# Kernel optimization log

Hardware: AMD Instinct MI355X
Metric: run time of the kernel (lower is better)

Reference implementation:

```python
import jax, jax.numpy as jnp
import numpy as np


def setup_inputs() -> dict:
    key = jax.random.key(0)
    ks = jax.random.split(key, 8)
    B, A = 2048, 64
    STATE, ACT = 5, 4
    d_in = STATE + ACT  # 9
    x = jax.random.normal(ks[0], (B, STATE), dtype=jnp.float32)
    actions = jax.random.normal(ks[1], (A, ACT), dtype=jnp.float32)
    def lin(k, fin, fout):
        return jax.random.normal(k, (fin, fout), dtype=jnp.float32) / np.sqrt(fin)
    W1 = lin(ks[2], d_in, 128); b1 = jnp.zeros((128,), jnp.float32)
    W2 = lin(ks[3], 128, 1024); b2 = jnp.zeros((1024,), jnp.float32)
    W3 = lin(ks[4], 1024, 1024); b3 = jnp.zeros((1024,), jnp.float32)
    W4 = lin(ks[5], 1024, 128); b4 = jnp.zeros((128,), jnp.float32)
    W5 = lin(ks[6], 128, 1); b5 = jnp.zeros((1,), jnp.float32)
    return {"x": x, "actions": actions,
            "W1": W1, "b1": b1, "W2": W2, "b2": b2, "W3": W3, "b3": b3,
            "W4": W4, "b4": b4, "W5": W5, "b5": b5}


def reference(x, actions, W1, b1, W2, b2, W3, b3, W4, b4, W5, b5):
    # x: [B,5] states; actions: [A,4] candidate actions.
    # Equivalent to the original's per-sample per-action loop: evaluate the
    # 5-layer Tanh MLP on concat(state, action) for every (sample, action) pair.
    B = x.shape[0]
    A = actions.shape[0]
    s = jnp.broadcast_to(x[:, None, :], (B, A, x.shape[1]))
    a = jnp.broadcast_to(actions[None, :, :], (B, A, actions.shape[1]))
    inp = jnp.concatenate([s, a], axis=-1)  # [B,A,9]
    h = jnp.tanh(inp @ W1 + b1)
    h = jnp.tanh(h @ W2 + b2)
    h = jnp.tanh(h @ W3 + b3)
    h = jnp.tanh(h @ W4 + b4)
    values = (h @ W5 + b5)[..., 0]  # [B,A]
    best = jnp.argmax(values, axis=1)  # [B]
    max_value_action = actions[best]  # [B,4]
    return (max_value_action, values)
```

## Files before the change

kernel.cpp:

```cpp
#include <hip/hip_runtime.h>
#include <hip/hip_bf16.h>
#include <math.h>


typedef short bf16x8 __attribute__((ext_vector_type(8)));
typedef float f32x4 __attribute__((ext_vector_type(4)));
typedef float f32x16 __attribute__((ext_vector_type(16)));

__device__ __host__ inline unsigned short f2bf(float f) {
    union { float f; unsigned u; } v; v.f = f;
    unsigned r = v.u + 0x7fff + ((v.u >> 16) & 1);
    return (unsigned short)(r >> 16);
}
__device__ inline unsigned short cvt_bf16(float f) {
    __hip_bfloat16 h = __float2bfloat16(f);
    return *reinterpret_cast<unsigned short*>(&h);
}
__device__ inline float bf2f(unsigned short b) {
    union { unsigned u; float f; } v; v.u = ((unsigned)b) << 16;
    return v.f;
}
__device__ inline float fast_tanh(float x) {
    float e = __expf(2.0f * x);
    return 1.0f - 2.0f * __builtin_amdgcn_rcpf(e + 1.0f);
}

#define DELTA 0.025f
#define WL_CAP 4096

struct WLE { unsigned long long mask; unsigned s; unsigned pad; };

#define HSWZ(row, b) ((b) ^ (((row) & 15) << 4))

__global__ __launch_bounds__(256) void pack_all(
    const float* __restrict__ W2, const float* __restrict__ W3, const float* __restrict__ W4,
    unsigned short* __restrict__ W2p, unsigned short* __restrict__ W3p,
    unsigned short* __restrict__ W4p, unsigned* __restrict__ wl_cnt)
{
    int tid = blockIdx.x * 256 + threadIdx.x;
    if (tid == 0) *wl_cnt = 0u;
    int blob = tid >> 6, lane = tid & 63;
    if (blob >= 2560) return;
    bf16x8 v;
    if (blob < 256) {
        int nt = blob >> 2, kt = blob & 3;
        int n = nt * 16 + (lane & 15);
        int kbase = kt * 32 + ((lane >> 4) & 3) * 8;
        #pragma unroll
        for (int e = 0; e < 8; ++e) v[e] = (short)f2bf(W2[(size_t)(kbase + e) * 1024 + n]);
        *(bf16x8*)&W2p[(size_t)blob * 512 + lane * 8] = v;
    } else if (blob < 2304) {
        int lb = blob - 256;
        int nt = lb >> 6, kt = lb & 63;
        int n = nt * 32 + (lane & 31);
        int kbase = kt * 16 + (lane >> 5) * 8;
        #pragma unroll
        for (int e = 0; e < 8; ++e) v[e] = (short)f2bf(W3[(size_t)(kbase + e) * 1024 + n]);
        *(bf16x8*)&W3p[(size_t)lb * 512 + lane * 8] = v;
    } else {
        int lb = blob - 2304;
        int nt = lb >> 5, kt = lb & 31;
        int n = nt * 16 + (lane & 15);
        int kbase = kt * 32 + ((lane >> 4) & 3) * 8;
        #pragma unroll
        for (int e = 0; e < 8; ++e) v[e] = (short)f2bf(W4[(size_t)(kbase + e) * 128 + n]);
        *(bf16x8*)&W4p[(size_t)lb * 512 + lane * 8] = v;
    }
}

__global__ __launch_bounds__(1024, 4) void qnet_mfma(
    const float* __restrict__ x, const float* __restrict__ actions,
    const float* __restrict__ W1, const float* __restrict__ b1,
    const float* __restrict__ b2, const float* __restrict__ b3,
    const float* __restrict__ b4,
    const float* __restrict__ W5, const float* __restrict__ b5,
    const unsigned short* __restrict__ W2p,
    const unsigned short* __restrict__ W3p,
    const unsigned short* __restrict__ W4p,
    float* __restrict__ values)
{
    __shared__ unsigned short h2b[2][64 * 256];
    __shared__ unsigned short hc[64 * 128];

    const int t = threadIdx.x;
    const int lane = t & 63;
    const int wave = t >> 6;
    const int p0 = blockIdx.x * 64;
    const int l15 = lane & 15;
    const int kb16 = (lane >> 4) * 16;
    const int kb32 = (lane >> 5) * 16;

    {
        int r = t >> 4;
        int c0 = (t & 15) * 8;
        const float* xs = &x[blockIdx.x * 5];
        const float* as = &actions[r * 4];
        float in[9] = { xs[0], xs[1], xs[2], xs[3], xs[4], as[0], as[1], as[2], as[3] };
        #pragma unroll
        for (int j = 0; j < 8; ++j) {
            int c = c0 + j;
            float acc = b1[c];
            #pragma unroll
            for (int k = 0; k < 9; ++k) acc += in[k] * W1[k * 128 + c];
            *(unsigned short*)((char*)hc + r * 256 + HSWZ(r, c * 2)) = cvt_bf16(fast_tanh(acc));
        }
    }
    __syncthreads();

    auto layer2_chunk = [&](int c, int buf) {
        const int nT = c * 16 + wave;
        const float bv = b2[nT * 16 + l15];
        char* bufp = (char*)&h2b[buf][0];
        const int lcb = (nT & 15) * 32 + l15 * 2;
        #pragma unroll 1
        for (int rt = 0; rt < 4; ++rt) {
            f32x4 acc = (f32x4){ bv, bv, bv, bv };
            const int row = rt * 16 + l15;
            #pragma unroll
            for (int ks = 0; ks < 4; ++ks) {
                bf16x8 b = *(const bf16x8*)((const char*)W2p + (nT * 4 + ks) * 1024 + lane * 16);
                bf16x8 a = *(const bf16x8*)((const char*)hc + row * 256 + HSWZ(row, ks * 64 + kb16));
                acc = __builtin_amdgcn_mfma_f32_16x16x32_bf16(a, b, acc, 0, 0, 0);
            }
            #pragma unroll
            for (int rr = 0; rr < 4; ++rr) {
                int m = rt * 16 + (lane >> 4) * 4 + rr;
                *(unsigned short*)(bufp + m * 512 + HSWZ(m, lcb)) = cvt_bf16(fast_tanh(acc[rr]));
            }
        }
    };

    f32x16 a00, a01, a10, a11;
    {
        float bv0 = b3[wave * 64 + (lane & 31)];
        float bv1 = b3[wave * 64 + 32 + (lane & 31)];
        #pragma unroll
        for (int i = 0; i < 16; ++i) { a00[i] = bv0; a10[i] = bv0; a01[i] = bv1; a11[i] = bv1; }
    }

    layer2_chunk(0, 0);
    __syncthreads();

    const int r0 = lane & 31, r1 = 32 + (lane & 31);
    for (int c = 0; c < 4; ++c) {
        if (c < 3) layer2_chunk(c + 1, (c + 1) & 1);
        const char* buf = (const char*)&h2b[c & 1][0];
        const char* bb = (const char*)W3p + (wave * 128 + c * 16) * 1024 + lane * 16;
        #pragma unroll 2
        for (int kt = 0; kt < 16; ++kt) {
            bf16x8 A0 = *(const bf16x8*)(buf + r0 * 512 + HSWZ(r0, kt * 32 + kb32));
            bf16x8 A1 = *(const bf16x8*)(buf + r1 * 512 + HSWZ(r1, kt * 32 + kb32));
            bf16x8 B0 = *(const bf16x8*)(bb + kt * 1024);
            bf16x8 B1 = *(const bf16x8*)(bb + 65536 + kt * 1024);
            a00 = __builtin_amdgcn_mfma_f32_32x32x16_bf16(A0, B0, a00, 0, 0, 0);
            a10 = __builtin_amdgcn_mfma_f32_32x32x16_bf16(A1, B0, a10, 0, 0, 0);
            a01 = __builtin_amdgcn_mfma_f32_32x32x16_bf16(A0, B1, a01, 0, 0, 0);
            a11 = __builtin_amdgcn_mfma_f32_32x32x16_bf16(A1, B1, a11, 0, 0, 0);
        }
        __syncthreads();
    }

    char* stage = (char*)&h2b[0][0];
    const int ct = wave & 7, rtp = wave >> 3;
    const int c0b = (wave * 64 + (lane & 31)) * 2;
    const float bv4 = b4[ct * 16 + l15];

    #pragma unroll
    for (int h = 0; h < 2; ++h) {
        #pragma unroll
        for (int r = 0; r < 16; ++r) {
            int row = (r & 3) + 8 * (r >> 2) + 4 * (lane >> 5);
            float vlo = h ? a10[r] : a00[r];
            float vhi = h ? a11[r] : a01[r];
            *(unsigned short*)(stage + row * 2048 + HSWZ(row, c0b)) = cvt_bf16(fast_tanh(vlo));
            *(unsigned short*)(stage + row * 2048 + HSWZ(row, c0b + 64)) = cvt_bf16(fast_tanh(vhi));
        }
        __syncthreads();
        f32x4 acc4 = (f32x4){ bv4, bv4, bv4, bv4 };
        const int rowL = rtp * 16 + l15;
        #pragma unroll 4
        for (int k32 = 0; k32 < 32; ++k32) {
            bf16x8 B = *(const bf16x8*)((const char*)W4p + (ct * 32 + k32) * 1024 + lane * 16);
            bf16x8 a = *(const bf16x8*)(stage + rowL * 2048 + HSWZ(rowL, k32 * 64 + kb16));
            acc4 = __builtin_amdgcn_mfma_f32_16x16x32_bf16(a, B, acc4, 0, 0, 0);
        }
        int n = ct * 16 + l15;
        #pragma unroll
        for (int rr = 0; rr < 4; ++rr) {
            int m = h * 32 + rtp * 16 + (lane >> 4) * 4 + rr;
            *(unsigned short*)((char*)hc + m * 256 + HSWZ(m, n * 2)) = cvt_bf16(fast_tanh(acc4[rr]));
        }
        __syncthreads();
    }

    {
        int r = t >> 4, g = t & 15;
        float part = 0.0f;
        #pragma unroll
        for (int j = 0; j < 8; ++j) {
            int cidx = g * 8 + j;
            unsigned short hb = *(const unsigned short*)((const char*)hc + r * 256 + HSWZ(r, cidx * 2));
            part += bf2f(hb) * W5[cidx];
        }
        part += __shfl_down(part, 8);
        part += __shfl_down(part, 4);
        part += __shfl_down(part, 2);
        part += __shfl_down(part, 1);
        if (g == 0) values[p0 + r] = part + b5[0];
    }
}

__global__ __launch_bounds__(256) void scan_argmax(
    const float* __restrict__ values, const float* __restrict__ actions,
    float* __restrict__ out_actions, unsigned* __restrict__ wl_cnt,
    WLE* __restrict__ wl)
{
    int wave = threadIdx.x >> 6, lane = threadIdx.x & 63;
    int s = blockIdx.x * 4 + wave;
    float myv = values[s * 64 + lane];
    float v = myv; int idx = lane;
    #pragma unroll
    for (int off = 32; off; off >>= 1) {
        float ov = __shfl_down(v, off);
        int oi = __shfl_down(idx, off);
        if (ov > v || (ov == v && oi < idx)) { v = ov; idx = oi; }
    }
    float vm = __shfl(v, 0);
    int best = __shfl(idx, 0);
    unsigned long long mask = __ballot(myv >= vm - DELTA);
    if (lane == 0 && __popcll(mask) > 1) {
        unsigned slot = atomicAdd(wl_cnt, 1u);
        if (slot < WL_CAP) { wl[slot].mask = mask; wl[slot].s = (unsigned)s; }
    }
    if (lane < 4) out_actions[s * 4 + lane] = actions[best * 4 + lane];
}

__global__ __launch_bounds__(256) void fixup_eval(
    const float* __restrict__ x, const float* __restrict__ actions,
    const float* __restrict__ W1, const float* __restrict__ b1,
    const float* __restrict__ W2, const float* __restrict__ b2,
    const float* __restrict__ W3, const float* __restrict__ b3,
    const float* __restrict__ W4, const float* __restrict__ b4,
    const float* __restrict__ W5, const float* __restrict__ b5,
    const unsigned* __restrict__ wl_cnt, const WLE* __restrict__ wl,
    float* __restrict__ out_actions)
{
    __shared__ float h1s[8][128];
    __shared__ float h2s[8][1024];
    __shared__ float h3s[8][1024];
    __shared__ float h4s[8][128];
    __shared__ float ain[8][4];
    __shared__ float xs[5];
    __shared__ int cand[64];
    __shared__ int ncand;
    __shared__ float vals[8];
    __shared__ float bestv; __shared__ int besti;

    const int t = threadIdx.x;
    int n = (int)*wl_cnt;
    if (n > WL_CAP) n = WL_CAP;
    for (int e = blockIdx.x; e < n; e += gridDim.x) {
        unsigned long long mask = wl[e].mask;
        int s = (int)wl[e].s;
        if (t == 0) {
            int nn = 0; unsigned long long m2 = mask;
            while (m2) { cand[nn++] = __ffsll(m2) - 1; m2 &= m2 - 1; }
            ncand = nn; bestv = -1e30f; besti = 0;
        }
        if (t < 5) xs[t] = x[s * 5 + t];
        __syncthreads();
        const int NC = ncand;
        for (int g = 0; g < NC; g += 8) {
            if (t < 32) {
                int rr = t >> 2;
                int src = (g + rr < NC) ? cand[g + rr] : cand[g];
                ain[rr][t & 3] = actions[src * 4 + (t & 3)];
            }
            __syncthreads();
            {
                int r = t >> 5, cb = (t & 31) * 4;
                #pragma unroll
                for (int j = 0; j < 4; ++j) {
                    int c = cb + j;
                    float acc = b1[c];
                    #pragma unroll
                    for (int k = 0; k < 5; ++k) acc += xs[k] * W1[k * 128 + c];
                    #pragma unroll
                    for (int k = 0; k < 4; ++k) acc += ain[r][k] * W1[(5 + k) * 128 + c];
                    h1s[r][c] = tanhf(acc);
                }
            }
            __syncthreads();
            {
                int cb = t * 4;
                float acc[8][4];
                float4 bv = *(const float4*)&b2[cb];
                #pragma unroll
                for (int r = 0; r < 8; ++r) { acc[r][0]=bv.x; acc[r][1]=bv.y; acc[r][2]=bv.z; acc[r][3]=bv.w; }
                for (int k = 0; k < 128; ++k) {
                    float4 w = *(const float4*)&W2[k * 1024 + cb];
                    #pragma unroll
                    for (int r = 0; r < 8; ++r) {
                        float hv = h1s[r][k];
                        acc[r][0] += hv * w.x; acc[r][1] += hv * w.y;
                        acc[r][2] += hv * w.z; acc[r][3] += hv * w.w;
                    }
                }
                #pragma unroll
                for (int r = 0; r < 8; ++r) {
                    h2s[r][cb+0] = tanhf(acc[r][0]); h2s[r][cb+1] = tanhf(acc[r][1]);
                    h2s[r][cb+2] = tanhf(acc[r][2]); h2s[r][cb+3] = tanhf(acc[r][3]);
                }
            }
            __syncthreads();
            {
                int cb = t * 4;
                float acc[8][4];
                float4 bv = *(const float4*)&b3[cb];
                #pragma unroll
                for (int r = 0; r < 8; ++r) { acc[r][0]=bv.x; acc[r][1]=bv.y; acc[r][2]=bv.z; acc[r][3]=bv.w; }
                for (int k = 0; k < 1024; ++k) {
                    float4 w = *(const float4*)&W3[k * 1024 + cb];
                    #pragma unroll
                    for (int r = 0; r < 8; ++r) {
                        float hv = h2s[r][k];
                        acc[r][0] += hv * w.x; acc[r][1] += hv * w.y;
                        acc[r][2] += hv * w.z; acc[r][3] += hv * w.w;
                    }
                }
                #pragma unroll
                for (int r = 0; r < 8; ++r) {
                    h3s[r][cb+0] = tanhf(acc[r][0]); h3s[r][cb+1] = tanhf(acc[r][1]);
                    h3s[r][cb+2] = tanhf(acc[r][2]); h3s[r][cb+3] = tanhf(acc[r][3]);
                }
            }
            __syncthreads();
            {
                int r = t >> 5, cb = (t & 31) * 4;
                float acc[4];
                float4 bv = *(const float4*)&b4[cb];
                acc[0]=bv.x; acc[1]=bv.y; acc[2]=bv.z; acc[3]=bv.w;
                for (int k = 0; k < 1024; ++k) {
                    float4 w = *(const float4*)&W4[k * 128 + cb];
                    float hv = h3s[r][k];
                    acc[0] += hv * w.x; acc[1] += hv * w.y; acc[2] += hv * w.z; acc[3] += hv * w.w;
                }
                h4s[r][cb+0] = tanhf(acc[0]); h4s[r][cb+1] = tanhf(acc[1]);
                h4s[r][cb+2] = tanhf(acc[2]); h4s[r][cb+3] = tanhf(acc[3]);
            }
            __syncthreads();
            if (t < 8) {
                float acc = b5[0];
                for (int k = 0; k < 128; ++k) acc += h4s[t][k] * W5[k];
                vals[t] = acc;
            }
            __syncthreads();
            if (t == 0) {
                int lim = (NC - g < 8) ? (NC - g) : 8;
                for (int i = 0; i < lim; ++i)
                    if (vals[i] > bestv) { bestv = vals[i]; besti = cand[g + i]; }
            }
            __syncthreads();
        }
        if (t < 4) out_actions[s * 4 + t] = actions[besti * 4 + t];
        __syncthreads();
    }
}

#define TR 16
__global__ __launch_bounds__(256) void qnet_fused(
    const float* __restrict__ x, const float* __restrict__ actions,
    const float* __restrict__ W1, const float* __restrict__ b1,
    const float* __restrict__ W2, const float* __restrict__ b2,
    const float* __restrict__ W3, const float* __restrict__ b3,
    const float* __restrict__ W4, const float* __restrict__ b4,
    const float* __restrict__ W5, const float* __restrict__ b5,
    float* __restrict__ values)
{
    __shared__ float h_small[TR][128];
    __shared__ float hA[TR][1024];
    __shared__ float hB[TR][1024];
    const int t = threadIdx.x;
    const int p0 = blockIdx.x * TR;
    for (int i = t; i < TR * 128; i += 256) {
        int r = i >> 7, c = i & 127;
        int p = p0 + r;
        int bidx = p >> 6, aidx = p & 63;
        float acc = b1[c];
        for (int k = 0; k < 5; ++k) acc += x[bidx * 5 + k] * W1[k * 128 + c];
        for (int k = 0; k < 4; ++k) acc += actions[aidx * 4 + k] * W1[(5 + k) * 128 + c];
        h_small[r][c] = tanhf(acc);
    }
    __syncthreads();
    {
        const int c0 = t * 4;
        float4 bias = *(const float4*)&b2[c0];
        float acc[TR][4];
        for (int r = 0; r < TR; ++r) { acc[r][0]=bias.x; acc[r][1]=bias.y; acc[r][2]=bias.z; acc[r][3]=bias.w; }
        for (int k = 0; k < 128; k += 4) {
            float4 w0 = *(const float4*)&W2[(k+0)*1024+c0];
            float4 w1 = *(const float4*)&W2[(k+1)*1024+c0];
            float4 w2 = *(const float4*)&W2[(k+2)*1024+c0];
            float4 w3 = *(const float4*)&W2[(k+3)*1024+c0];
            for (int r = 0; r < TR; ++r) {
                float4 hv = *(const float4*)&h_small[r][k];
                acc[r][0] += hv.x*w0.x + hv.y*w1.x + hv.z*w2.x + hv.w*w3.x;
                acc[r][1] += hv.x*w0.y + hv.y*w1.y + hv.z*w2.y + hv.w*w3.y;
                acc[r][2] += hv.x*w0.z + hv.y*w1.z + hv.z*w2.z + hv.w*w3.z;
                acc[r][3] += hv.x*w0.w + hv.y*w1.w + hv.z*w2.w + hv.w*w3.w;
            }
        }
        for (int r = 0; r < TR; ++r) {
            hA[r][c0+0]=tanhf(acc[r][0]); hA[r][c0+1]=tanhf(acc[r][1]);
            hA[r][c0+2]=tanhf(acc[r][2]); hA[r][c0+3]=tanhf(acc[r][3]);
        }
    }
    __syncthreads();
    {
        const int c0 = t * 4;
        float4 bias = *(const float4*)&b3[c0];
        float acc[TR][4];
        for (int r = 0; r < TR; ++r) { acc[r][0]=bias.x; acc[r][1]=bias.y; acc[r][2]=bias.z; acc[r][3]=bias.w; }
        for (int k = 0; k < 1024; k += 4) {
            float4 w0 = *(const float4*)&W3[(k+0)*1024+c0];
            float4 w1 = *(const float4*)&W3[(k+1)*1024+c0];
            float4 w2 = *(const float4*)&W3[(k+2)*1024+c0];
            float4 w3 = *(const float4*)&W3[(k+3)*1024+c0];
            for (int r = 0; r < TR; ++r) {
                float4 hv = *(const float4*)&hA[r][k];
                acc[r][0] += hv.x*w0.x + hv.y*w1.x + hv.z*w2.x + hv.w*w3.x;
                acc[r][1] += hv.x*w0.y + hv.y*w1.y + hv.z*w2.y + hv.w*w3.y;
                acc[r][2] += hv.x*w0.z + hv.y*w1.z + hv.z*w2.z + hv.w*w3.z;
                acc[r][3] += hv.x*w0.w + hv.y*w1.w + hv.z*w2.w + hv.w*w3.w;
            }
        }
        for (int r = 0; r < TR; ++r) {
            hB[r][c0+0]=tanhf(acc[r][0]); hB[r][c0+1]=tanhf(acc[r][1]);
            hB[r][c0+2]=tanhf(acc[r][2]); hB[r][c0+3]=tanhf(acc[r][3]);
        }
    }
    __syncthreads();
    {
        const int c = t & 127;
        const int rh = t >> 7;
        float acc[8];
        float bias = b4[c];
        for (int r = 0; r < 8; ++r) acc[r] = bias;
        for (int k = 0; k < 1024; k += 4) {
            float w0 = W4[(k+0)*128+c], w1 = W4[(k+1)*128+c];
            float w2 = W4[(k+2)*128+c], w3 = W4[(k+3)*128+c];
            for (int r = 0; r < 8; ++r) {
                float4 hv = *(const float4*)&hB[rh*8+r][k];
                acc[r] += hv.x*w0 + hv.y*w1 + hv.z*w2 + hv.w*w3;
            }
        }
        for (int r = 0; r < 8; ++r) h_small[rh*8+r][c] = tanhf(acc[r]);
    }
    __syncthreads();
    if (t < TR) {
        float acc = b5[0];
        for (int k = 0; k < 128; k += 4) {
            float4 hv = *(const float4*)&h_small[t][k];
            float4 wv = *(const float4*)&W5[k];
            acc += hv.x*wv.x + hv.y*wv.y + hv.z*wv.z + hv.w*wv.w;
        }
        values[p0 + t] = acc;
    }
}

__global__ __launch_bounds__(256) void argmax_gather(
    const float* __restrict__ values, const float* __restrict__ actions,
    float* __restrict__ out_actions)
{
    const int wave = threadIdx.x >> 6;
    const int lane = threadIdx.x & 63;
    const int state = blockIdx.x * (blockDim.x >> 6) + wave;
    float v = values[state * 64 + lane];
    int idx = lane;
    for (int off = 32; off; off >>= 1) {
        float ov = __shfl_down(v, off);
        int oi = __shfl_down(idx, off);
        if (ov > v || (ov == v && oi < idx)) { v = ov; idx = oi; }
    }
    idx = __shfl(idx, 0);
    if (lane < 4) out_actions[state * 4 + lane] = actions[idx * 4 + lane];
}

extern "C" void kernel_launch(void* const* d_in, const int* in_sizes, int n_in,
                              void* d_out, int out_size, void* d_ws, size_t ws_size,
                              hipStream_t stream) {
    const float* x       = (const float*)d_in[0];
    const float* actions = (const float*)d_in[1];
    const float* W1 = (const float*)d_in[2];  const float* b1 = (const float*)d_in[3];
    const float* W2 = (const float*)d_in[4];  const float* b2 = (const float*)d_in[5];
    const float* W3 = (const float*)d_in[6];  const float* b3 = (const float*)d_in[7];
    const float* W4 = (const float*)d_in[8];  const float* b4 = (const float*)d_in[9];
    const float* W5 = (const float*)d_in[10]; const float* b5 = (const float*)d_in[11];

    float* out_actions = (float*)d_out;
    float* values      = (float*)d_out + 2048 * 4;

    const size_t nW2 = 128 * 1024, nW3 = 1024 * 1024, nW4 = 1024 * 128;
    const size_t wbytes = (nW2 + nW3 + nW4) * sizeof(unsigned short);
    const size_t need = wbytes + 16 + (size_t)WL_CAP * sizeof(WLE);

    if (ws_size >= need) {
        unsigned short* W2p = (unsigned short*)d_ws;
        unsigned short* W3p = W2p + nW2;
        unsigned short* W4p = W3p + nW3;
        unsigned* wl_cnt = (unsigned*)((char*)d_ws + wbytes);
        WLE* wl = (WLE*)((char*)d_ws + wbytes + 16);

        pack_all<<<640, 256, 0, stream>>>(W2, W3, W4, W2p, W3p, W4p, wl_cnt);
        qnet_mfma<<<2048, 1024, 0, stream>>>(x, actions, W1, b1, b2, b3, b4, W5, b5,
                                             W2p, W3p, W4p, values);
        scan_argmax<<<512, 256, 0, stream>>>(values, actions, out_actions, wl_cnt, wl);
        fixup_eval<<<512, 256, 0, stream>>>(x, actions, W1, b1, W2, b2, W3, b3,
                                            W4, b4, W5, b5, wl_cnt, wl, out_actions);
    } else {
        qnet_fused<<<2048 * 64 / TR, 256, 0, stream>>>(x, actions, W1, b1, W2, b2, W3, b3,
                                                       W4, b4, W5, b5, values);
        argmax_gather<<<2048 / 4, 256, 0, stream>>>(values, actions, out_actions);
    }
}
```

Measured before the change: 643.6 us.

## Halve qnet block to 512 threads, split layer3 into two passes, rework fixup

The main MFMA kernel now uses 8 waves instead of 16. Each wave computes two layer-2 column tiles, and layer 3 runs in two output-column passes. Layer 4 partial sums accumulate across both passes, so layer 2 is computed twice per block. This frees LDS staging space and could allow higher occupancy per CU, and s_setprio is added around the layer-3 MFMA loop. In exchange, each wave does more serial work and layer 2 is redundantly recomputed. The fixup kernel is also changed to 1024-thread blocks with one output column per thread.

```diff
diff --git a/kernel.cpp b/kernel.cpp
--- a/kernel.cpp
+++ b/kernel.cpp
@@ -68,7 +68,7 @@
     }
 }
 
-__global__ __launch_bounds__(1024, 4) void qnet_mfma(
+__global__ __launch_bounds__(512, 4) void qnet_mfma(
     const float* __restrict__ x, const float* __restrict__ actions,
     const float* __restrict__ W1, const float* __restrict__ b1,
     const float* __restrict__ b2, const float* __restrict__ b3,
@@ -79,25 +79,25 @@
     const unsigned short* __restrict__ W4p,
     float* __restrict__ values)
 {
-    __shared__ unsigned short h2b[2][64 * 256];
+    __shared__ unsigned short h2b[2 * 64 * 256];
     __shared__ unsigned short hc[64 * 128];
 
     const int t = threadIdx.x;
     const int lane = t & 63;
-    const int wave = t >> 6;
+    const int w = t >> 6;
     const int p0 = blockIdx.x * 64;
     const int l15 = lane & 15;
     const int kb16 = (lane >> 4) * 16;
     const int kb32 = (lane >> 5) * 16;
 
     {
-        int r = t >> 4;
-        int c0 = (t & 15) * 8;
+        int r = t >> 3;
+        int c0 = (t & 7) * 16;
         const float* xs = &x[blockIdx.x * 5];
         const float* as = &actions[r * 4];
         float in[9] = { xs[0], xs[1], xs[2], xs[3], xs[4], as[0], as[1], as[2], as[3] };
-        #pragma unroll
-        for (int j = 0; j < 8; ++j) {
+        #pragma unroll 4
+        for (int j = 0; j < 16; ++j) {
             int c = c0 + j;
             float acc = b1[c];
             #pragma unroll
@@ -107,102 +107,133 @@
     }
     __syncthreads();
 
-    auto layer2_chunk = [&](int c, int buf) {
-        const int nT = c * 16 + wave;
-        const float bv = b2[nT * 16 + l15];
-        char* bufp = (char*)&h2b[buf][0];
-        const int lcb = (nT & 15) * 32 + l15 * 2;
+    auto layer2_chunk = [&](int c, int b) {
+        char* bufp = (char*)h2b + b * 32768;
+        #pragma unroll
+        for (int j = 0; j < 2; ++j) {
+            const int nT = c * 16 + w * 2 + j;
+            const float bv = b2[nT * 16 + l15];
+            const int lcb = ((w * 2 + j) * 16 + l15) * 2;
+            #pragma unroll 1
+            for (int rt = 0; rt < 4; ++rt) {
+                f32x4 acc = (f32x4){ bv, bv, bv, bv };
+                const int row = rt * 16 + l15;
+                #pragma unroll
+                for (int ks = 0; ks < 4; ++ks) {
+                    bf16x8 bfr = *(const bf16x8*)((const char*)W2p + (nT * 4 + ks) * 1024 + lane * 16);
+                    bf16x8 a = *(const bf16x8*)((const char*)hc + row * 256 + HSWZ(row, ks * 64 + kb16));
+                    acc = __builtin_amdgcn_mfma_f32_16x16x32_bf16(a, bfr, acc, 0, 0, 0);
+                }
+                #pragma unroll
+                for (int rr = 0; rr < 4; ++rr) {
+                    int m = rt * 16 + (lane >> 4) * 4 + rr;
+                    *(unsigned short*)(bufp + m * 512 + HSWZ(m, lcb)) = cvt_bf16(fast_tanh(acc[rr]));
+                }
+            }
+        }
+    };
+
+    f32x4 acc4[4];
+    {
+        const float bv4 = b4[w * 16 + l15];
+        #pragma unroll
+        for (int rt = 0; rt < 4; ++rt) acc4[rt] = (f32x4){ bv4, bv4, bv4, bv4 };
+    }
+
+    layer2_chunk(0, 0);
+    __syncthreads();
+
+    const int r0 = lane & 31, r1 = 32 + (lane & 31);
+
+    #pragma unroll 1
+    for (int p = 0; p < 2; ++p) {
+        f32x16 a00, a01, a10, a11;
+        {
+            float bv0 = b3[p * 512 + w * 64 + (lane & 31)];
+            float bv1 = b3[p * 512 + w * 64 + 32 + (lane & 31)];
+            #pragma unroll
+            for (int i = 0; i < 16; ++i) { a00[i] = bv0; a10[i] = bv0; a01[i] = bv1; a11[i] = bv1; }
+        }
+        const int bbase = ((p * 16 + w * 2) * 64) * 1024 + lane * 16;
+
         #pragma unroll 1
-        for (int rt = 0; rt < 4; ++rt) {
-            f32x4 acc = (f32x4){ bv, bv, bv, bv };
-            const int row = rt * 16 + l15;
+        for (int c = 0; c < 4; ++c) {
+            if (c < 3) layer2_chunk(c + 1, (c + 1) & 1);
+            const char* bufp = (const char*)h2b + (c & 1) * 32768;
+            const char* bb = (const char*)W3p + bbase + c * 16384;
+            __builtin_amdgcn_s_setprio(1);
+            #pragma unroll 2
+            for (int kt = 0; kt < 16; ++kt) {
+                bf16x8 A0 = *(const bf16x8*)(bufp + r0 * 512 + HSWZ(r0, kt * 32 + kb32));
+                bf16x8 A1 = *(const bf16x8*)(bufp + r1 * 512 + HSWZ(r1, kt * 32 + kb32));
+                bf16x8 B0 = *(const bf16x8*)(bb + kt * 1024);
+                bf16x8 B1 = *(const bf16x8*)(bb + 65536 + kt * 1024);
+                a00 = __builtin_amdgcn_mfma_f32_32x32x16_bf16(A0, B0, a00, 0, 0, 0);
+                a10 = __builtin_amdgcn_mfma_f32_32x32x16_bf16(A1, B0, a10, 0, 0, 0);
+                a01 = __builtin_amdgcn_mfma_f32_32x32x16_bf16(A0, B1, a01, 0, 0, 0);
+                a11 = __builtin_amdgcn_mfma_f32_32x32x16_bf16(A1, B1, a11, 0, 0, 0);
+            }
+            __builtin_amdgcn_s_setprio(0);
+            __syncthreads();
+        }
+
+        {
+            char* stage = (char*)h2b;
+            const int lc0 = (w * 64 + (lane & 31)) * 2;
             #pragma unroll
-            for (int ks = 0; ks < 4; ++ks) {
-                bf16x8 b = *(const bf16x8*)((const char*)W2p + (nT * 4 + ks) * 1024 + lane * 16);
-                bf16x8 a = *(const bf16x8*)((const char*)hc + row * 256 + HSWZ(row, ks * 64 + kb16));
-                acc = __builtin_amdgcn_mfma_f32_16x16x32_bf16(a, b, acc, 0, 0, 0);
-            }
+            for (int r = 0; r < 16; ++r) {
+                int row = (r & 3) + 8 * (r >> 2) + 4 * (lane >> 5);
+                int rowB = row + 32;
+                *(unsigned short*)(stage + row  * 1024 + HSWZ(row,  lc0)) = cvt_bf16(fast_tanh(a00[r]));
+                *(unsigned short*)(stage + rowB * 1024 + HSWZ(rowB, lc0)) = cvt_bf16(fast_tanh(a10[r]));
+                *(unsigned short*)(stage + row  * 1024 + HSWZ(row,  lc0 + 64)) = cvt_bf16(fast_tanh(a01[r]));
+                *(unsigned short*)(stage + rowB * 1024 + HSWZ(rowB, lc0 + 64)) = cvt_bf16(fast_tanh(a11[r]));
+            }
+        }
+        __syncthreads();
+
+        {
+            const char* stage = (const char*)h2b;
+            #pragma unroll 2
+            for (int kg = 0; kg < 16; ++kg) {
+                bf16x8 B = *(const bf16x8*)((const char*)W4p + (w * 32 + p * 16 + kg) * 1024 + lane * 16);
+                #pragma unroll
+                for (int rt = 0; rt < 4; ++rt) {
+                    int row = rt * 16 + l15;
+                    bf16x8 a = *(const bf16x8*)(stage + row * 1024 + HSWZ(row, kg * 64 + kb16));
+                    acc4[rt] = __builtin_amdgcn_mfma_f32_16x16x32_bf16(a, B, acc4[rt], 0, 0, 0);
+                }
+            }
+        }
+        __syncthreads();
+
+        if (p == 0) {
+            layer2_chunk(0, 0);
+            __syncthreads();
+        }
+    }
+
+    {
+        int n = w * 16 + l15;
+        #pragma unroll
+        for (int rt = 0; rt < 4; ++rt)
             #pragma unroll
             for (int rr = 0; rr < 4; ++rr) {
                 int m = rt * 16 + (lane >> 4) * 4 + rr;
-                *(unsigned short*)(bufp + m * 512 + HSWZ(m, lcb)) = cvt_bf16(fast_tanh(acc[rr]));
-            }
-        }
-    };
-
-    f32x16 a00, a01, a10, a11;
-    {
-        float bv0 = b3[wave * 64 + (lane & 31)];
-        float bv1 = b3[wave * 64 + 32 + (lane & 31)];
-        #pragma unroll
-        for (int i = 0; i < 16; ++i) { a00[i] = bv0; a10[i] = bv0; a01[i] = bv1; a11[i] = bv1; }
-    }
-
-    layer2_chunk(0, 0);
-    __syncthreads();
-
-    const int r0 = lane & 31, r1 = 32 + (lane & 31);
-    for (int c = 0; c < 4; ++c) {
-        if (c < 3) layer2_chunk(c + 1, (c + 1) & 1);
-        const char* buf = (const char*)&h2b[c & 1][0];
-        const char* bb = (const char*)W3p + (wave * 128 + c * 16) * 1024 + lane * 16;
-        #pragma unroll 2
-        for (int kt = 0; kt < 16; ++kt) {
-            bf16x8 A0 = *(const bf16x8*)(buf + r0 * 512 + HSWZ(r0, kt * 32 + kb32));
-            bf16x8 A1 = *(const bf16x8*)(buf + r1 * 512 + HSWZ(r1, kt * 32 + kb32));
-            bf16x8 B0 = *(const bf16x8*)(bb + kt * 1024);
-            bf16x8 B1 = *(const bf16x8*)(bb + 65536 + kt * 1024);
-            a00 = __builtin_amdgcn_mfma_f32_32x32x16_bf16(A0, B0, a00, 0, 0, 0);
-            a10 = __builtin_amdgcn_mfma_f32_32x32x16_bf16(A1, B0, a10, 0, 0, 0);
-            a01 = __builtin_amdgcn_mfma_f32_32x32x16_bf16(A0, B1, a01, 0, 0, 0);
-            a11 = __builtin_amdgcn_mfma_f32_32x32x16_bf16(A1, B1, a11, 0, 0, 0);
-        }
-        __syncthreads();
-    }
-
-    char* stage = (char*)&h2b[0][0];
-    const int ct = wave & 7, rtp = wave >> 3;
-    const int c0b = (wave * 64 + (lane & 31)) * 2;
-    const float bv4 = b4[ct * 16 + l15];
-
-    #pragma unroll
-    for (int h = 0; h < 2; ++h) {
-        #pragma unroll
-        for (int r = 0; r < 16; ++r) {
-            int row = (r & 3) + 8 * (r >> 2) + 4 * (lane >> 5);
-            float vlo = h ? a10[r] : a00[r];
-            float vhi = h ? a11[r] : a01[r];
-            *(unsigned short*)(stage + row * 2048 + HSWZ(row, c0b)) = cvt_bf16(fast_tanh(vlo));
-            *(unsigned short*)(stage + row * 2048 + HSWZ(row, c0b + 64)) = cvt_bf16(fast_tanh(vhi));
-        }
-        __syncthreads();
-        f32x4 acc4 = (f32x4){ bv4, bv4, bv4, bv4 };
-        const int rowL = rtp * 16 + l15;
-        #pragma unroll 4
-        for (int k32 = 0; k32 < 32; ++k32) {
-            bf16x8 B = *(const bf16x8*)((const char*)W4p + (ct * 32 + k32) * 1024 + lane * 16);
-            bf16x8 a = *(const bf16x8*)(stage + rowL * 2048 + HSWZ(rowL, k32 * 64 + kb16));
-            acc4 = __builtin_amdgcn_mfma_f32_16x16x32_bf16(a, B, acc4, 0, 0, 0);
-        }
-        int n = ct * 16 + l15;
-        #pragma unroll
-        for (int rr = 0; rr < 4; ++rr) {
-            int m = h * 32 + rtp * 16 + (lane >> 4) * 4 + rr;
-            *(unsigned short*)((char*)hc + m * 256 + HSWZ(m, n * 2)) = cvt_bf16(fast_tanh(acc4[rr]));
-        }
-        __syncthreads();
-    }
-
-    {
-        int r = t >> 4, g = t & 15;
+                *(unsigned short*)((char*)hc + m * 256 + HSWZ(m, n * 2)) = cvt_bf16(fast_tanh(acc4[rt][rr]));
+            }
+    }
+    __syncthreads();
+
+    {
+        int r = t >> 3, g = t & 7;
         float part = 0.0f;
         #pragma unroll
-        for (int j = 0; j < 8; ++j) {
-            int cidx = g * 8 + j;
+        for (int j = 0; j < 16; ++j) {
+            int cidx = g * 16 + j;
             unsigned short hb = *(const unsigned short*)((const char*)hc + r * 256 + HSWZ(r, cidx * 2));
             part += bf2f(hb) * W5[cidx];
         }
-        part += __shfl_down(part, 8);
         part += __shfl_down(part, 4);
         part += __shfl_down(part, 2);
         part += __shfl_down(part, 1);
@@ -235,7 +266,7 @@
     if (lane < 4) out_actions[s * 4 + lane] = actions[best * 4 + lane];
 }
 
-__global__ __launch_bounds__(256) void fixup_eval(
+__global__ __launch_bounds__(1024) void fixup_eval(
     const float* __restrict__ x, const float* __restrict__ actions,
     const float* __restrict__ W1, const float* __restrict__ b1,
     const float* __restrict__ W2, const float* __restrict__ b2,
@@ -278,75 +309,50 @@
             }
             __syncthreads();
             {
-                int r = t >> 5, cb = (t & 31) * 4;
-                #pragma unroll
-                for (int j = 0; j < 4; ++j) {
-                    int c = cb + j;
-                    float acc = b1[c];
+                int r = t >> 7, c = t & 127;
+                float acc = b1[c];
+                #pragma unroll
+                for (int k = 0; k < 5; ++k) acc += xs[k] * W1[k * 128 + c];
+                #pragma unroll
+                for (int k = 0; k < 4; ++k) acc += ain[r][k] * W1[(5 + k) * 128 + c];
+                h1s[r][c] = tanhf(acc);
+            }
+            __syncthreads();
+            {
+                int c = t;
+                float acc[8];
+                float bv = b2[c];
+                #pragma unroll
+                for (int r = 0; r < 8; ++r) acc[r] = bv;
+                for (int k = 0; k < 128; ++k) {
+                    float wv = W2[k * 1024 + c];
                     #pragma unroll
-                    for (int k = 0; k < 5; ++k) acc += xs[k] * W1[k * 128 + c];
+                    for (int r = 0; r < 8; ++r) acc[r] += h1s[r][k] * wv;
+                }
+                #pragma unroll
+                for (int r = 0; r < 8; ++r) h2s[r][c] = tanhf(acc[r]);
+            }
+            __syncthreads();
+            {
+                int c = t;
+                float acc[8];
+                float bv = b3[c];
+                #pragma unroll
+                for (int r = 0; r < 8; ++r) acc[r] = bv;
+                for (int k = 0; k < 1024; ++k) {
+                    float wv = W3[k * 1024 + c];
                     #pragma unroll
-                    for (int k = 0; k < 4; ++k) acc += ain[r][k] * W1[(5 + k) * 128 + c];
-                    h1s[r][c] = tanhf(acc);
+                    for (int r = 0; r < 8; ++r) acc[r] += h2s[r][k] * wv;
                 }
+                #pragma unroll
+                for (int r = 0; r < 8; ++r) h3s[r][c] = tanhf(acc[r]);
             }
             __syncthreads();
             {
-                int cb = t * 4;
-                float acc[8][4];
-                float4 bv = *(const float4*)&b2[cb];
-                #pragma unroll
-                for (int r = 0; r < 8; ++r) { acc[r][0]=bv.x; acc[r][1]=bv.y; acc[r][2]=bv.z; acc[r][3]=bv.w; }
-                for (int k = 0; k < 128; ++k) {
-                    float4 w = *(const float4*)&W2[k * 1024 + cb];
-                    #pragma unroll
-                    for (int r = 0; r < 8; ++r) {
-                        float hv = h1s[r][k];
-                        acc[r][0] += hv * w.x; acc[r][1] += hv * w.y;
-                        acc[r][2] += hv * w.z; acc[r][3] += hv * w.w;
-                    }
-                }
-                #pragma unroll
-                for (int r = 0; r < 8; ++r) {
-                    h2s[r][cb+0] = tanhf(acc[r][0]); h2s[r][cb+1] = tanhf(acc[r][1]);
-                    h2s[r][cb+2] = tanhf(acc[r][2]); h2s[r][cb+3] = tanhf(acc[r][3]);
-                }
-            }
-            __syncthreads();
-            {
-                int cb = t * 4;
-                float acc[8][4];
-                float4 bv = *(const float4*)&b3[cb];
-                #pragma unroll
-                for (int r = 0; r < 8; ++r) { acc[r][0]=bv.x; acc[r][1]=bv.y; acc[r][2]=bv.z; acc[r][3]=bv.w; }
-                for (int k = 0; k < 1024; ++k) {
-                    float4 w = *(const float4*)&W3[k * 1024 + cb];
-                    #pragma unroll
-                    for (int r = 0; r < 8; ++r) {
-                        float hv = h2s[r][k];
-                        acc[r][0] += hv * w.x; acc[r][1] += hv * w.y;
-                        acc[r][2] += hv * w.z; acc[r][3] += hv * w.w;
-                    }
-                }
-                #pragma unroll
-                for (int r = 0; r < 8; ++r) {
-                    h3s[r][cb+0] = tanhf(acc[r][0]); h3s[r][cb+1] = tanhf(acc[r][1]);
-                    h3s[r][cb+2] = tanhf(acc[r][2]); h3s[r][cb+3] = tanhf(acc[r][3]);
-                }
-            }
-            __syncthreads();
-            {
-                int r = t >> 5, cb = (t & 31) * 4;
-                float acc[4];
-                float4 bv = *(const float4*)&b4[cb];
-                acc[0]=bv.x; acc[1]=bv.y; acc[2]=bv.z; acc[3]=bv.w;
-                for (int k = 0; k < 1024; ++k) {
-                    float4 w = *(const float4*)&W4[k * 128 + cb];
-                    float hv = h3s[r][k];
-                    acc[0] += hv * w.x; acc[1] += hv * w.y; acc[2] += hv * w.z; acc[3] += hv * w.w;
-                }
-                h4s[r][cb+0] = tanhf(acc[0]); h4s[r][cb+1] = tanhf(acc[1]);
-                h4s[r][cb+2] = tanhf(acc[2]); h4s[r][cb+3] = tanhf(acc[3]);
+                int r = t >> 7, c = t & 127;
+                float acc = b4[c];
+                for (int k = 0; k < 1024; ++k) acc += h3s[r][k] * W4[k * 128 + c];
+                h4s[r][c] = tanhf(acc);
             }
             __syncthreads();
             if (t < 8) {
@@ -512,11 +518,11 @@
         WLE* wl = (WLE*)((char*)d_ws + wbytes + 16);
 
         pack_all<<<640, 256, 0, stream>>>(W2, W3, W4, W2p, W3p, W4p, wl_cnt);
-        qnet_mfma<<<2048, 1024, 0, stream>>>(x, actions, W1, b1, b2, b3, b4, W5, b5,
-                                             W2p, W3p, W4p, values);
+        qnet_mfma<<<2048, 512, 0, stream>>>(x, actions, W1, b1, b2, b3, b4, W5, b5,
+                                            W2p, W3p, W4p, values);
         scan_argmax<<<512, 256, 0, stream>>>(values, actions, out_actions, wl_cnt, wl);
-        fixup_eval<<<512, 256, 0, stream>>>(x, actions, W1, b1, W2, b2, W3, b3,
-                                            W4, b4, W5, b5, wl_cnt, wl, out_actions);
+        fixup_eval<<<256, 1024, 0, stream>>>(x, actions, W1, b1, W2, b2, W3, b3,
+                                             W4, b4, W5, b5, wl_cnt, wl, out_actions);
     } else {
         qnet_fused<<<2048 * 64 / TR, 256, 0, stream>>>(x, actions, W1, b1, W2, b2, W3, b3,
                                                        W4, b4, W5, b5, values);
```

Result: slower. 900.3 us (+39.9%).

## Fuse argmax into MFMA kernel, flatten fixup work items, stagger layer2/layer3 by wave group

Applied to the files above, without the earlier changes.

Moves the per-sample argmax and near-tie detection into the main MFMA kernel, removing the separate scan kernel and its reread of values. Near-tie candidates become flat per-(sample,action) items evaluated in batches of 8 by the fp32 fixup kernel, and a new finalize kernel picks the best per sample. This replaces the old one-sample-per-block fixup, which wasted rows when a sample had few candidates. The main loop also has half the waves do layer-3 MFMA before the layer-2 chunk, raising priority around the MFMAs so the two phases overlap. It adds a kernel launch and atomics, and samples are silently skipped when the item capacity is exceeded.

```diff
diff --git a/kernel.cpp b/kernel.cpp
--- a/kernel.cpp
+++ b/kernel.cpp
@@ -26,19 +26,19 @@
 }
 
 #define DELTA 0.025f
-#define WL_CAP 4096
-
-struct WLE { unsigned long long mask; unsigned s; unsigned pad; };
+#define ITEM_CAP 16384
+
+struct WLE { unsigned s, base, nc, pad; };
 
 #define HSWZ(row, b) ((b) ^ (((row) & 15) << 4))
 
 __global__ __launch_bounds__(256) void pack_all(
     const float* __restrict__ W2, const float* __restrict__ W3, const float* __restrict__ W4,
     unsigned short* __restrict__ W2p, unsigned short* __restrict__ W3p,
-    unsigned short* __restrict__ W4p, unsigned* __restrict__ wl_cnt)
+    unsigned short* __restrict__ W4p, unsigned* __restrict__ cnts)
 {
     int tid = blockIdx.x * 256 + threadIdx.x;
-    if (tid == 0) *wl_cnt = 0u;
+    if (tid < 2) cnts[tid] = 0u;
     int blob = tid >> 6, lane = tid & 63;
     if (blob >= 2560) return;
     bf16x8 v;
@@ -77,7 +77,9 @@
     const unsigned short* __restrict__ W2p,
     const unsigned short* __restrict__ W3p,
     const unsigned short* __restrict__ W4p,
-    float* __restrict__ values)
+    float* __restrict__ values, float* __restrict__ out_actions,
+    unsigned* __restrict__ cnts, WLE* __restrict__ wl,
+    unsigned* __restrict__ items)
 {
     __shared__ unsigned short h2b[2][64 * 256];
     __shared__ unsigned short hc[64 * 128];
@@ -85,6 +87,7 @@
     const int t = threadIdx.x;
     const int lane = t & 63;
     const int wave = t >> 6;
+    const int grp = (wave >> 2) & 1;
     const int p0 = blockIdx.x * 64;
     const int l15 = lane & 15;
     const int kb16 = (lane >> 4) * 16;
@@ -111,7 +114,7 @@
         const int nT = c * 16 + wave;
         const float bv = b2[nT * 16 + l15];
         char* bufp = (char*)&h2b[buf][0];
-        const int lcb = (nT & 15) * 32 + l15 * 2;
+        const int lcb = (wave * 16 + l15) * 2;
         #pragma unroll 1
         for (int rt = 0; rt < 4; ++rt) {
             f32x4 acc = (f32x4){ bv, bv, bv, bv };
@@ -137,25 +140,36 @@
         #pragma unroll
         for (int i = 0; i < 16; ++i) { a00[i] = bv0; a10[i] = bv0; a01[i] = bv1; a11[i] = bv1; }
     }
-
-    layer2_chunk(0, 0);
-    __syncthreads();
-
     const int r0 = lane & 31, r1 = 32 + (lane & 31);
-    for (int c = 0; c < 4; ++c) {
-        if (c < 3) layer2_chunk(c + 1, (c + 1) & 1);
-        const char* buf = (const char*)&h2b[c & 1][0];
+
+    auto l3_step = [&](int c) {
+        const char* bufp = (const char*)&h2b[c & 1][0];
         const char* bb = (const char*)W3p + (wave * 128 + c * 16) * 1024 + lane * 16;
+        __builtin_amdgcn_s_setprio(1);
         #pragma unroll 2
         for (int kt = 0; kt < 16; ++kt) {
-            bf16x8 A0 = *(const bf16x8*)(buf + r0 * 512 + HSWZ(r0, kt * 32 + kb32));
-            bf16x8 A1 = *(const bf16x8*)(buf + r1 * 512 + HSWZ(r1, kt * 32 + kb32));
+            bf16x8 A0 = *(const bf16x8*)(bufp + r0 * 512 + HSWZ(r0, kt * 32 + kb32));
+            bf16x8 A1 = *(const bf16x8*)(bufp + r1 * 512 + HSWZ(r1, kt * 32 + kb32));
             bf16x8 B0 = *(const bf16x8*)(bb + kt * 1024);
             bf16x8 B1 = *(const bf16x8*)(bb + 65536 + kt * 1024);
             a00 = __builtin_amdgcn_mfma_f32_32x32x16_bf16(A0, B0, a00, 0, 0, 0);
             a10 = __builtin_amdgcn_mfma_f32_32x32x16_bf16(A1, B0, a10, 0, 0, 0);
             a01 = __builtin_amdgcn_mfma_f32_32x32x16_bf16(A0, B1, a01, 0, 0, 0);
             a11 = __builtin_amdgcn_mfma_f32_32x32x16_bf16(A1, B1, a11, 0, 0, 0);
+        }
+        __builtin_amdgcn_s_setprio(0);
+    };
+
+    layer2_chunk(0, 0);
+    __syncthreads();
+
+    for (int c = 0; c < 4; ++c) {
+        if (grp == 0) {
+            if (c < 3) layer2_chunk(c + 1, (c + 1) & 1);
+            l3_step(c);
+        } else {
+            l3_step(c);
+            if (c < 3) layer2_chunk(c + 1, (c + 1) & 1);
         }
         __syncthreads();
     }
@@ -193,6 +207,7 @@
         __syncthreads();
     }
 
+    float* vbuf = (float*)&h2b[0][0];
     {
         int r = t >> 4, g = t & 15;
         float part = 0.0f;
@@ -206,33 +221,44 @@
         part += __shfl_down(part, 4);
         part += __shfl_down(part, 2);
         part += __shfl_down(part, 1);
-        if (g == 0) values[p0 + r] = part + b5[0];
-    }
-}
-
-__global__ __launch_bounds__(256) void scan_argmax(
-    const float* __restrict__ values, const float* __restrict__ actions,
-    float* __restrict__ out_actions, unsigned* __restrict__ wl_cnt,
-    WLE* __restrict__ wl)
-{
-    int wave = threadIdx.x >> 6, lane = threadIdx.x & 63;
-    int s = blockIdx.x * 4 + wave;
-    float myv = values[s * 64 + lane];
-    float v = myv; int idx = lane;
-    #pragma unroll
-    for (int off = 32; off; off >>= 1) {
-        float ov = __shfl_down(v, off);
-        int oi = __shfl_down(idx, off);
-        if (ov > v || (ov == v && oi < idx)) { v = ov; idx = oi; }
-    }
-    float vm = __shfl(v, 0);
-    int best = __shfl(idx, 0);
-    unsigned long long mask = __ballot(myv >= vm - DELTA);
-    if (lane == 0 && __popcll(mask) > 1) {
-        unsigned slot = atomicAdd(wl_cnt, 1u);
-        if (slot < WL_CAP) { wl[slot].mask = mask; wl[slot].s = (unsigned)s; }
-    }
-    if (lane < 4) out_actions[s * 4 + lane] = actions[best * 4 + lane];
+        if (g == 0) {
+            float val = part + b5[0];
+            values[p0 + r] = val;
+            vbuf[r] = val;
+        }
+    }
+    __syncthreads();
+
+    if (t < 64) {
+        float myv = vbuf[t];
+        float v = myv; int idx = t;
+        #pragma unroll
+        for (int off = 32; off; off >>= 1) {
+            float ov = __shfl_down(v, off);
+            int oi = __shfl_down(idx, off);
+            if (ov > v || (ov == v && oi < idx)) { v = ov; idx = oi; }
+        }
+        float vm = __shfl(v, 0);
+        int best = __shfl(idx, 0);
+        if (t < 4) out_actions[blockIdx.x * 4 + t] = actions[best * 4 + t];
+        unsigned long long mask = __ballot(myv >= vm - DELTA);
+        int nc = __popcll(mask);
+        if (nc > 1) {
+            unsigned base = 0;
+            if (t == 0) base = atomicAdd(&cnts[1], (unsigned)nc);
+            base = (unsigned)__shfl((int)base, 0);
+            if (base + (unsigned)nc <= (unsigned)ITEM_CAP) {
+                if (t == 0) {
+                    unsigned slot = atomicAdd(&cnts[0], 1u);
+                    wl[slot].s = blockIdx.x; wl[slot].base = base; wl[slot].nc = (unsigned)nc;
+                }
+                if (myv >= vm - DELTA) {
+                    int rank = __popcll(mask & ((1ull << t) - 1ull));
+                    items[base + rank] = ((unsigned)blockIdx.x << 6) | (unsigned)t;
+                }
+            }
+        }
+    }
 }
 
 __global__ __launch_bounds__(256) void fixup_eval(
@@ -242,129 +268,133 @@
     const float* __restrict__ W3, const float* __restrict__ b3,
     const float* __restrict__ W4, const float* __restrict__ b4,
     const float* __restrict__ W5, const float* __restrict__ b5,
-    const unsigned* __restrict__ wl_cnt, const WLE* __restrict__ wl,
-    float* __restrict__ out_actions)
+    const unsigned* __restrict__ cnts, const unsigned* __restrict__ items,
+    float* __restrict__ vexact)
 {
     __shared__ float h1s[8][128];
     __shared__ float h2s[8][1024];
     __shared__ float h3s[8][1024];
     __shared__ float h4s[8][128];
+    __shared__ float xin[8][5];
     __shared__ float ain[8][4];
-    __shared__ float xs[5];
-    __shared__ int cand[64];
-    __shared__ int ncand;
-    __shared__ float vals[8];
-    __shared__ float bestv; __shared__ int besti;
 
     const int t = threadIdx.x;
-    int n = (int)*wl_cnt;
-    if (n > WL_CAP) n = WL_CAP;
-    for (int e = blockIdx.x; e < n; e += gridDim.x) {
-        unsigned long long mask = wl[e].mask;
-        int s = (int)wl[e].s;
-        if (t == 0) {
-            int nn = 0; unsigned long long m2 = mask;
-            while (m2) { cand[nn++] = __ffsll(m2) - 1; m2 &= m2 - 1; }
-            ncand = nn; bestv = -1e30f; besti = 0;
-        }
-        if (t < 5) xs[t] = x[s * 5 + t];
-        __syncthreads();
-        const int NC = ncand;
-        for (int g = 0; g < NC; g += 8) {
-            if (t < 32) {
-                int rr = t >> 2;
-                int src = (g + rr < NC) ? cand[g + rr] : cand[g];
-                ain[rr][t & 3] = actions[src * 4 + (t & 3)];
-            }
-            __syncthreads();
-            {
-                int r = t >> 5, cb = (t & 31) * 4;
+    int n = (int)cnts[1]; if (n > ITEM_CAP) n = ITEM_CAP;
+    int nb = (n + 7) >> 3;
+    for (int b = blockIdx.x; b < nb; b += gridDim.x) {
+        if (t < 8) {
+            int idx = b * 8 + t;
+            unsigned it = items[(idx < n) ? idx : (b * 8)];
+            int s = (int)((it >> 6) & 2047), a = (int)(it & 63);
+            #pragma unroll
+            for (int k = 0; k < 5; ++k) xin[t][k] = x[s * 5 + k];
+            #pragma unroll
+            for (int k = 0; k < 4; ++k) ain[t][k] = actions[a * 4 + k];
+        }
+        __syncthreads();
+        {
+            int r = t >> 5, cb = (t & 31) * 4;
+            #pragma unroll
+            for (int j = 0; j < 4; ++j) {
+                int c = cb + j;
+                float acc = b1[c];
                 #pragma unroll
-                for (int j = 0; j < 4; ++j) {
-                    int c = cb + j;
-                    float acc = b1[c];
-                    #pragma unroll
-                    for (int k = 0; k < 5; ++k) acc += xs[k] * W1[k * 128 + c];
-                    #pragma unroll
-                    for (int k = 0; k < 4; ++k) acc += ain[r][k] * W1[(5 + k) * 128 + c];
-                    h1s[r][c] = tanhf(acc);
-                }
-            }
-            __syncthreads();
-            {
-                int cb = t * 4;
-                float acc[8][4];
-                float4 bv = *(const float4*)&b2[cb];
+                for (int k = 0; k < 5; ++k) acc += xin[r][k] * W1[k * 128 + c];
                 #pragma unroll
-                for (int r = 0; r < 8; ++r) { acc[r][0]=bv.x; acc[r][1]=bv.y; acc[r][2]=bv.z; acc[r][3]=bv.w; }
-                for (int k = 0; k < 128; ++k) {
-                    float4 w = *(const float4*)&W2[k * 1024 + cb];
-                    #pragma unroll
-                    for (int r = 0; r < 8; ++r) {
-                        float hv = h1s[r][k];
-                        acc[r][0] += hv * w.x; acc[r][1] += hv * w.y;
-                        acc[r][2] += hv * w.z; acc[r][3] += hv * w.w;
-                    }
-                }
+                for (int k = 0; k < 4; ++k) acc += ain[r][k] * W1[(5 + k) * 128 + c];
+                h1s[r][c] = tanhf(acc);
+            }
+        }
+        __syncthreads();
+        {
+            int cb = t * 4;
+            float acc[8][4];
+            float4 bv = *(const float4*)&b2[cb];
+            #pragma unroll
+            for (int r = 0; r < 8; ++r) { acc[r][0]=bv.x; acc[r][1]=bv.y; acc[r][2]=bv.z; acc[r][3]=bv.w; }
+            for (int k = 0; k < 128; ++k) {
+                float4 w = *(const float4*)&W2[k * 1024 + cb];
                 #pragma unroll
                 for (int r = 0; r < 8; ++r) {
-                    h2s[r][cb+0] = tanhf(acc[r][0]); h2s[r][cb+1] = tanhf(acc[r][1]);
-                    h2s[r][cb+2] = tanhf(acc[r][2]); h2s[r][cb+3] = tanhf(acc[r][3]);
+                    float hv = h1s[r][k];
+                    acc[r][0] += hv * w.x; acc[r][1] += hv * w.y;
+                    acc[r][2] += hv * w.z; acc[r][3] += hv * w.w;
                 }
             }
-            __syncthreads();
-            {
-                int cb = t * 4;
-                float acc[8][4];
-                float4 bv = *(const float4*)&b3[cb];
-                #pragma unroll
-                for (int r = 0; r < 8; ++r) { acc[r][0]=bv.x; acc[r][1]=bv.y; acc[r][2]=bv.z; acc[r][3]=bv.w; }
-                for (int k = 0; k < 1024; ++k) {
-                    float4 w = *(const float4*)&W3[k * 1024 + cb];
-                    #pragma unroll
-                    for (int r = 0; r < 8; ++r) {
-                        float hv = h2s[r][k];
-                        acc[r][0] += hv * w.x; acc[r][1] += hv * w.y;
-                        acc[r][2] += hv * w.z; acc[r][3] += hv * w.w;
-                    }
-                }
+            #pragma unroll
+            for (int r = 0; r < 8; ++r) {
+                h2s[r][cb+0] = tanhf(acc[r][0]); h2s[r][cb+1] = tanhf(acc[r][1]);
+                h2s[r][cb+2] = tanhf(acc[r][2]); h2s[r][cb+3] = tanhf(acc[r][3]);
+            }
+        }
+        __syncthreads();
+        {
+            int cb = t * 4;
+            float acc[8][4];
+            float4 bv = *(const float4*)&b3[cb];
+            #pragma unroll
+            for (int r = 0; r < 8; ++r) { acc[r][0]=bv.x; acc[r][1]=bv.y; acc[r][2]=bv.z; acc[r][3]=bv.w; }
+            for (int k = 0; k < 1024; ++k) {
+                float4 w = *(const float4*)&W3[k * 1024 + cb];
                 #pragma unroll
                 for (int r = 0; r < 8; ++r) {
-                    h3s[r][cb+0] = tanhf(acc[r][0]); h3s[r][cb+1] = tanhf(acc[r][1]);
-                    h3s[r][cb+2] = tanhf(acc[r][2]); h3s[r][cb+3] = tanhf(acc[r][3]);
+                    float hv = h2s[r][k];
+                    acc[r][0] += hv * w.x; acc[r][1] += hv * w.y;
+                    acc[r][2] += hv * w.z; acc[r][3] += hv * w.w;
                 }
             }
-            __syncthreads();
-            {
-                int r = t >> 5, cb = (t & 31) * 4;
-                float acc[4];
-                float4 bv = *(const float4*)&b4[cb];
-                acc[0]=bv.x; acc[1]=bv.y; acc[2]=bv.z; acc[3]=bv.w;
-                for (int k = 0; k < 1024; ++k) {
-                    float4 w = *(const float4*)&W4[k * 128 + cb];
-                    float hv = h3s[r][k];
-                    acc[0] += hv * w.x; acc[1] += hv * w.y; acc[2] += hv * w.z; acc[3] += hv * w.w;
-                }
-                h4s[r][cb+0] = tanhf(acc[0]); h4s[r][cb+1] = tanhf(acc[1]);
-                h4s[r][cb+2] = tanhf(acc[2]); h4s[r][cb+3] = tanhf(acc[3]);
-            }
-            __syncthreads();
-            if (t < 8) {
-                float acc = b5[0];
-                for (int k = 0; k < 128; ++k) acc += h4s[t][k] * W5[k];
-                vals[t] = acc;
-            }
-            __syncthreads();
-            if (t == 0) {
-                int lim = (NC - g < 8) ? (NC - g) : 8;
-                for (int i = 0; i < lim; ++i)
-                    if (vals[i] > bestv) { bestv = vals[i]; besti = cand[g + i]; }
-            }
-            __syncthreads();
-        }
-        if (t < 4) out_actions[s * 4 + t] = actions[besti * 4 + t];
-        __syncthreads();
-    }
+            #pragma unroll
+            for (int r = 0; r < 8; ++r) {
+                h3s[r][cb+0] = tanhf(acc[r][0]); h3s[r][cb+1] = tanhf(acc[r][1]);
+                h3s[r][cb+2] = tanhf(acc[r][2]); h3s[r][cb+3] = tanhf(acc[r][3]);
+            }
+        }
+        __syncthreads();
+        {
+            int r = t >> 5, cb = (t & 31) * 4;
+            float acc[4];
+            float4 bv = *(const float4*)&b4[cb];
+            acc[0]=bv.x; acc[1]=bv.y; acc[2]=bv.z; acc[3]=bv.w;
+            for (int k = 0; k < 1024; ++k) {
+                float4 w = *(const float4*)&W4[k * 128 + cb];
+                float hv = h3s[r][k];
+                acc[0] += hv * w.x; acc[1] += hv * w.y; acc[2] += hv * w.z; acc[3] += hv * w.w;
+            }
+            h4s[r][cb+0] = tanhf(acc[0]); h4s[r][cb+1] = tanhf(acc[1]);
+            h4s[r][cb+2] = tanhf(acc[2]); h4s[r][cb+3] = tanhf(acc[3]);
+        }
+        __syncthreads();
+        if (t < 8) {
+            float acc = b5[0];
+            for (int k = 0; k < 128; ++k) acc += h4s[t][k] * W5[k];
+            int idx = b * 8 + t;
+            if (idx < n) vexact[idx] = acc;
+        }
+        __syncthreads();
+    }
+}
+
+__global__ __launch_bounds__(256) void finalize_argmax(
+    const unsigned* __restrict__ cnts, const WLE* __restrict__ wl,
+    const unsigned* __restrict__ items, const float* __restrict__ vexact,
+    const float* __restrict__ actions, float* __restrict__ out_actions)
+{
+    int gw = (blockIdx.x * 256 + threadIdx.x) >> 6;
+    int lane = threadIdx.x & 63;
+    int nwl = (int)cnts[0]; if (nwl > 2048) nwl = 2048;
+    if (gw >= nwl) return;
+    unsigned s = wl[gw].s, base = wl[gw].base, nc = wl[gw].nc;
+    float v = (lane < (int)nc) ? vexact[base + lane] : -3.0e38f;
+    int idx = lane;
+    #pragma unroll
+    for (int off = 32; off; off >>= 1) {
+        float ov = __shfl_down(v, off);
+        int oi = __shfl_down(idx, off);
+        if (ov > v || (ov == v && oi < idx)) { v = ov; idx = oi; }
+    }
+    int i0 = __shfl(idx, 0);
+    int a = (int)(items[base + i0] & 63);
+    if (lane < 4) out_actions[s * 4 + lane] = actions[a * 4 + lane];
 }
 
 #define TR 16
@@ -502,21 +532,26 @@
 
     const size_t nW2 = 128 * 1024, nW3 = 1024 * 1024, nW4 = 1024 * 128;
     const size_t wbytes = (nW2 + nW3 + nW4) * sizeof(unsigned short);
-    const size_t need = wbytes + 16 + (size_t)WL_CAP * sizeof(WLE);
+    const size_t need = wbytes + 16 + 2048 * sizeof(WLE) + ITEM_CAP * 4 + ITEM_CAP * 4;
 
     if (ws_size >= need) {
         unsigned short* W2p = (unsigned short*)d_ws;
         unsigned short* W3p = W2p + nW2;
         unsigned short* W4p = W3p + nW3;
-        unsigned* wl_cnt = (unsigned*)((char*)d_ws + wbytes);
-        WLE* wl = (WLE*)((char*)d_ws + wbytes + 16);
-
-        pack_all<<<640, 256, 0, stream>>>(W2, W3, W4, W2p, W3p, W4p, wl_cnt);
+        char* p = (char*)d_ws + wbytes;
+        unsigned* cnts = (unsigned*)p;                 p += 16;
+        WLE* wl = (WLE*)p;                             p += 2048 * sizeof(WLE);
+        unsigned* items = (unsigned*)p;                p += ITEM_CAP * 4;
+        float* vexact = (float*)p;
+
+        pack_all<<<640, 256, 0, stream>>>(W2, W3, W4, W2p, W3p, W4p, cnts);
         qnet_mfma<<<2048, 1024, 0, stream>>>(x, actions, W1, b1, b2, b3, b4, W5, b5,
-                                             W2p, W3p, W4p, values);
-        scan_argmax<<<512, 256, 0, stream>>>(values, actions, out_actions, wl_cnt, wl);
+                                             W2p, W3p, W4p, values, out_actions,
+                                             cnts, wl, items);
         fixup_eval<<<512, 256, 0, stream>>>(x, actions, W1, b1, W2, b2, W3, b3,
-                                            W4, b4, W5, b5, wl_cnt, wl, out_actions);
+                                            W4, b4, W5, b5, cnts, items, vexact);
+        finalize_argmax<<<512, 256, 0, stream>>>(cnts, wl, items, vexact,
+                                                 actions, out_actions);
     } else {
         qnet_fused<<<2048 * 64 / TR, 256, 0, stream>>>(x, actions, W1, b1, W2, b2, W3, b3,
                                                        W4, b4, W5, b5, values);
```

Result: faster. 622.0 us (-3.4%).
